# Kernel optimization log

Measured on AMD Instinct MI355X. Metric: run time of the kernel, lower is better.

## Reference

```python
import jax, jax.numpy as jnp
import numpy as np

N, E, B = 50000, 800000, 64
F0, H, C = 8, 2, 64          # node feat dim, heads, per-head out dim
OBS, MH, NA = 128, 256, 16   # obs dim, mlp hidden, n_actions
NEG_SLOPE = 0.2


def setup_inputs() -> dict:
    key = jax.random.key(0)
    ks = jax.random.split(key, 30)
    p = lambda k, shape: (jax.random.normal(k, shape, dtype=jnp.float32) * 0.1)
    inp = {
        "obs": jax.random.normal(ks[0], (B, OBS), dtype=jnp.float32),
        "node_features": jax.random.normal(ks[1], (N, F0), dtype=jnp.float32),
        "edge_index": jax.random.randint(ks[2], (2, E), 0, N, dtype=jnp.int32),
        "batch": jnp.sort(jax.random.randint(ks[3], (N,), 0, B, dtype=jnp.int32)),
        # GAT layer 0: in=F0 -> heads=H, out=C, concat
        "W0": p(ks[4], (F0, H * C)), "a_src0": p(ks[5], (H, C)), "a_dst0": p(ks[6], (H, C)), "b0": p(ks[7], (H * C,)),
        # GAT layer 1: in=H*C -> heads=H, out=C, concat
        "W1": p(ks[8], (H * C, H * C)), "a_src1": p(ks[9], (H, C)), "a_dst1": p(ks[10], (H, C)), "b1": p(ks[11], (H * C,)),
        # GAT layer 2: in=H*C -> heads=1, out=C, no concat
        "W2": p(ks[12], (H * C, C)), "a_src2": p(ks[13], (1, C)), "a_dst2": p(ks[14], (1, C)), "b2": p(ks[15], (C,)),
        # MLP head: combined = C + OBS
        "Ws1": p(ks[16], (C + OBS, MH)), "bs1": p(ks[17], (MH,)),
        "ln_g": jnp.ones((MH,), jnp.float32), "ln_b": jnp.zeros((MH,), jnp.float32),
        "Ws2": p(ks[18], (MH, MH)), "bs2": p(ks[19], (MH,)),
        "Wa": p(ks[20], (MH, NA)), "ba": p(ks[21], (NA,)),
        "Wc": p(ks[22], (MH, 1)), "bc": p(ks[23], (1,)),
    }
    return inp


def gat_layer(x, src, dst, W, a_src, a_dst, bias, heads, out_dim, concat):
    n = x.shape[0]
    h = (x @ W).reshape(n, heads, out_dim)                     # [N,H,C]
    alpha_s = jnp.einsum("nhc,hc->nh", h, a_src)               # [N,H]
    alpha_d = jnp.einsum("nhc,hc->nh", h, a_dst)
    e = jax.nn.leaky_relu(alpha_s[src] + alpha_d[dst], NEG_SLOPE)  # [E,H]
    # scatter-softmax over incoming edges of each dst node (stable)
    emax = jax.ops.segment_max(e, dst, num_segments=n)
    ex = jnp.exp(e - emax[dst])
    denom = jax.ops.segment_sum(ex, dst, num_segments=n)
    alpha = ex / (denom[dst] + 1e-16)                          # [E,H]
    msg = h[src] * alpha[..., None]                            # [E,H,C]
    out = jax.ops.segment_sum(msg, dst, num_segments=n)        # [N,H,C]
    out = out.reshape(n, heads * out_dim) if concat else out.mean(axis=1)
    return out + bias


def reference(obs, node_features, edge_index, batch,
              W0, a_src0, a_dst0, b0, W1, a_src1, a_dst1, b1,
              W2, a_src2, a_dst2, b2,
              Ws1, bs1, ln_g, ln_b, Ws2, bs2, Wa, ba, Wc, bc):
    n = node_features.shape[0]
    # PyG GATConv default add_self_loops=True
    loop = jnp.arange(n, dtype=edge_index.dtype)
    src = jnp.concatenate([edge_index[0], loop])
    dst = jnp.concatenate([edge_index[1], loop])

    x = node_features
    x = jax.nn.elu(gat_layer(x, src, dst, W0, a_src0, a_dst0, b0, H, C, True))
    x = jax.nn.elu(gat_layer(x, src, dst, W1, a_src1, a_dst1, b1, H, C, True))
    x = gat_layer(x, src, dst, W2, a_src2, a_dst2, b2, 1, C, False)

    # global mean pool over graphs
    counts = jax.ops.segment_sum(jnp.ones((n,), x.dtype), batch, num_segments=B)
    pooled = jax.ops.segment_sum(x, batch, num_segments=B) / jnp.maximum(counts, 1.0)[:, None]

    combined = jnp.concatenate([pooled, obs], axis=-1)         # [B, C+OBS]
    h = combined @ Ws1 + bs1
    mu = h.mean(-1, keepdims=True)
    var = ((h - mu) ** 2).mean(-1, keepdims=True)
    h = (h - mu) / jnp.sqrt(var + 1e-5) * ln_g + ln_b
    h = jax.nn.relu(h)
    h = jax.nn.relu(h @ Ws2 + bs2)
    logits = h @ Wa + ba
    value = (h @ Wc + bc).squeeze(-1)
    return logits, value
```

## Files before the change

### kernel.cpp

```cpp
#include <hip/hip_runtime.h>
#include <math.h>


#define LRELU(x) ((x) > 0.f ? (x) : 0.2f * (x))

typedef short bf16x8 __attribute__((ext_vector_type(8)));
typedef unsigned short u16x8 __attribute__((ext_vector_type(8)));
typedef float f32x4 __attribute__((ext_vector_type(4)));
typedef float f32x2 __attribute__((ext_vector_type(2)));

__device__ __forceinline__ unsigned short f2bf(float f) {
    unsigned int u = __float_as_uint(f);
    u = (u + 0x7fffu + ((u >> 16) & 1u)) >> 16;
    return (unsigned short)u;
}
__device__ __forceinline__ float bf2f(unsigned short u) {
    return __uint_as_float((unsigned int)u << 16);
}
__device__ __forceinline__ unsigned char f2fp8(float f) {
    return (unsigned char)(__builtin_amdgcn_cvt_pk_fp8_f32(f, f, 0, false) & 0xff);
}
__device__ __forceinline__ f32x2 fp8pair(unsigned int u) {
    return __builtin_amdgcn_cvt_pk_f32_fp8(u, false);
}


__global__ __launch_bounds__(256) void hist_t0_kernel(
    const int* __restrict__ dst, int* __restrict__ histT,
    int e, int G1, int NB, int n, int hist_blocks, int t0_blocks, int wp_blocks,
    const float* __restrict__ x, const float* __restrict__ W,
    const float* __restrict__ a_src, const float* __restrict__ a_dst,
    unsigned char* __restrict__ h, float* __restrict__ as_o,
    float* __restrict__ ad_o,
    const float* __restrict__ W1, const float* __restrict__ W2,
    unsigned short* __restrict__ Wf1, unsigned short* __restrict__ Wf2,
    const int* __restrict__ batch, int* __restrict__ gstart, int nGraphs) {
    __shared__ unsigned int hist[256];
    __shared__ float xs[2][8][8];
    const int t = threadIdx.x;
    if ((int)blockIdx.x < hist_blocks) {
        hist[t] = 0;
        __syncthreads();
        int base = blockIdx.x * 2048 + t * 8;
        int d[8];
        if (base + 8 <= e) {
            int4 x0 = *(const int4*)(dst + base);
            int4 x1 = *(const int4*)(dst + base + 4);
            d[0] = x0.x; d[1] = x0.y; d[2] = x0.z; d[3] = x0.w;
            d[4] = x1.x; d[5] = x1.y; d[6] = x1.z; d[7] = x1.w;
        } else {
#pragma unroll
            for (int j = 0; j < 8; j++) {
                int ij = base + j;
                d[j] = (ij < e) ? dst[ij] : -1;
            }
        }
#pragma unroll
        for (int j = 0; j < 8; j++) {
            if (d[j] >= 0) atomicAdd(&hist[d[j] >> 8], 1u);
        }
        __syncthreads();
        if (t < NB) histT[t * G1 + blockIdx.x] = (int)hist[t];
        return;
    }
    if ((int)blockIdx.x < hist_blocks + t0_blocks) {
        const int bid2 = blockIdx.x - hist_blocks;
        const int tid = t & 127;
        const int half = t >> 7;
        const int node0 = bid2 * 16 + half * 8;

        for (int idx = tid; idx < 64; idx += 128) {
            int ni = idx >> 3, k = idx & 7;
            int ng = node0 + ni;
            xs[half][ni][k] = (ng < n) ? x[(size_t)ng * 8 + k] : 0.f;
        }
        __syncthreads();

        float acc[8];
#pragma unroll
        for (int i = 0; i < 8; i++) acc[i] = 0.f;
#pragma unroll
        for (int k = 0; k < 8; k++) {
            float wk = W[k * 128 + tid];
#pragma unroll
            for (int i = 0; i < 8; i++) acc[i] += xs[half][i][k] * wk;
        }

        const int lane = tid & 63;
        const int head = tid >> 6;
        const int pos = 2 * lane + head;
        const float av = a_src[tid];
        const float dv = a_dst[tid];
#pragma unroll
        for (int i = 0; i < 8; i++) {
            int ng = node0 + i;
            if (ng >= n) break;
            h[(size_t)ng * 128 + pos] = f2fp8(acc[i]);
            float ps = acc[i] * av, pd = acc[i] * dv;
            for (int off = 32; off; off >>= 1) {
                ps += __shfl_xor(ps, off, 64);
                pd += __shfl_xor(pd, off, 64);
            }
            if (lane == 0) {
                as_o[ng * 2 + head] = ps;
                ad_o[ng * 2 + head] = pd;
            }
        }
        return;
    }
    if ((int)blockIdx.x < hist_blocks + t0_blocks + wp_blocks) {
        const int n1 = 8 * 4 * 64;
        const int n2 = 4 * 4 * 64;
        int gid = (blockIdx.x - hist_blocks - t0_blocks) * 256 + t;
        if (gid < n1) {
            int idx = gid;
            int lane = idx & 63, ts = idx >> 6;
            int s = ts & 3, tt = ts >> 2;
            int quad = lane >> 4, cn = lane & 15;
#pragma unroll
            for (int j = 0; j < 8; j++)
                Wf1[idx * 8 + j] = f2bf(W1[(s * 32 + quad * 8 + j) * 128 + tt * 16 + cn]);
        } else if (gid < n1 + n2) {
            int idx = gid - n1;
            int lane = idx & 63, ts = idx >> 6;
            int s = ts & 3, tt = ts >> 2;
            int quad = lane >> 4, cn = lane & 15;
#pragma unroll
            for (int j = 0; j < 8; j++)
                Wf2[idx * 8 + j] = f2bf(W2[(s * 32 + quad * 8 + j) * 64 + tt * 16 + cn]);
        }
        return;
    }
    int gid = (blockIdx.x - hist_blocks - t0_blocks - wp_blocks) * 256 + t;
    if (gid < n) {
        int bi = batch[gid];
        if (gid == 0) {
            for (int g = 0; g <= bi; g++) gstart[g] = 0;
        } else {
            int bp = batch[gid - 1];
            if (bi != bp)
                for (int g = bp + 1; g <= bi; g++) gstart[g] = gid;
        }
        if (gid == n - 1) {
            for (int g = bi + 1; g <= nGraphs; g++) gstart[g] = n;
        }
    }
}


__global__ __launch_bounds__(256) void scan2_block_kernel(
    const int* __restrict__ in, int* __restrict__ out,
    int* __restrict__ blockSums, int len) {
    __shared__ int lds[256];
    int t = threadIdx.x;
    int i0 = blockIdx.x * 512 + 2 * t;
    int v0 = (i0 < len) ? in[i0] : 0;
    int v1 = (i0 + 1 < len) ? in[i0 + 1] : 0;
    int s = v0 + v1;
    lds[t] = s;
    __syncthreads();
    for (int off = 1; off < 256; off <<= 1) {
        int u = (t >= off) ? lds[t - off] : 0;
        __syncthreads();
        lds[t] += u;
        __syncthreads();
    }
    int base = lds[t] - s;
    if (i0 < len) out[i0] = base;
    if (i0 + 1 < len) out[i0 + 1] = base + v0;
    if (t == 255) blockSums[blockIdx.x] = lds[255];
}

__global__ __launch_bounds__(256) void scan2_finalize_kernel(
    int* __restrict__ out, const int* __restrict__ blockSums, int len, int nb) {
    __shared__ int lds[256];
    int t = threadIdx.x;
    int v = (t < nb) ? blockSums[t] : 0;
    lds[t] = v;
    __syncthreads();
    for (int off = 1; off < 256; off <<= 1) {
        int u = (t >= off) ? lds[t - off] : 0;
        __syncthreads();
        lds[t] += u;
        __syncthreads();
    }
    const int bid = blockIdx.x;
    const int base = (bid > 0) ? lds[bid - 1] : 0;
    const int total = lds[nb - 1];
    int i0 = bid * 512 + 2 * t;
#pragma unroll
    for (int q = 0; q < 2; q++) {
        int i = i0 + q;
        if (i < len) out[i] += base;
        else if (i == len) out[len] = total;
    }
}


__global__ __launch_bounds__(256) void bucket_scatter_kernel(
    const int* __restrict__ src, const int* __restrict__ dst,
    const int* __restrict__ offs, int* __restrict__ esrc,
    unsigned char* __restrict__ dsub8, int e, int G1, int NB) {
    __shared__ unsigned int hist[256];
    __shared__ int baseL[256];
    const int t = threadIdx.x;
    hist[t] = 0;
    if (t < NB) baseL[t] = offs[t * G1 + blockIdx.x];
    __syncthreads();
    int base = blockIdx.x * 2048 + t * 8;
    int d[8], s[8];
    if (base + 8 <= e) {
        int4 d0 = *(const int4*)(dst + base);
        int4 d1 = *(const int4*)(dst + base + 4);
        int4 s0 = *(const int4*)(src + base);
        int4 s1 = *(const int4*)(src + base + 4);
        d[0] = d0.x; d[1] = d0.y; d[2] = d0.z; d[3] = d0.w;
        d[4] = d1.x; d[5] = d1.y; d[6] = d1.z; d[7] = d1.w;
        s[0] = s0.x; s[1] = s0.y; s[2] = s0.z; s[3] = s0.w;
        s[4] = s1.x; s[5] = s1.y; s[6] = s1.z; s[7] = s1.w;
    } else {
#pragma unroll
        for (int j = 0; j < 8; j++) {
            int ij = base + j;
            bool v = ij < e;
            d[j] = v ? dst[ij] : -1;
            s[j] = v ? src[ij] : 0;
        }
    }
    unsigned lr[8];
#pragma unroll
    for (int j = 0; j < 8; j++) {
        lr[j] = (d[j] >= 0) ? atomicAdd(&hist[d[j] >> 8], 1u) : 0u;
    }
#pragma unroll
    for (int j = 0; j < 8; j++) {
        if (d[j] >= 0) {
            int pos = baseL[d[j] >> 8] + (int)lr[j];
            esrc[pos] = s[j];
            dsub8[pos] = (unsigned char)(d[j] & 255);
        }
    }
}


__global__ __launch_bounds__(256) void bucket_csr_kernel(
    const int* __restrict__ offs, const unsigned char* __restrict__ dsub8,
    const int* __restrict__ esrc, int* __restrict__ row_ptr,
    int* __restrict__ col, int G1, int n) {
    __shared__ unsigned int cnt[256];
    __shared__ int rp[256];
    int t = threadIdx.x;
    int b = blockIdx.x;
    cnt[t] = 0;
    __syncthreads();
    int bs = offs[b * G1];
    int be = offs[(b + 1) * G1];
    for (int i = bs + t; i < be; i += 256) {
        atomicAdd(&cnt[dsub8[i]], 1u);
    }
    __syncthreads();
    int v = (int)cnt[t];
    rp[t] = v;
    __syncthreads();
    for (int off = 1; off < 256; off <<= 1) {
        int u = (t >= off) ? rp[t - off] : 0;
        __syncthreads();
        rp[t] += u;
        __syncthreads();
    }
    int excl = rp[t] - v;
    int node = b * 256 + t;
    if (node <= n) row_ptr[node] = bs + excl;
    __syncthreads();
    cnt[t] = (unsigned)excl;
    __syncthreads();
    for (int i = bs + t; i < be; i += 256) {
        int sub = dsub8[i];
        unsigned r = atomicAdd(&cnt[sub], 1u);
        col[bs + (int)r] = esrc[i];
    }
}

template <int OUT, int HEADS>
__device__ __forceinline__ int hpos8(int c) {
    return (HEADS == 2) ? (2 * (c & 63) + (c >> 6)) : c;
}


template <int OUT, int HEADS>
__global__ __launch_bounds__(256) void transform_mfma_kernel(
    const unsigned short* __restrict__ xb, const unsigned short* __restrict__ Wf,
    const float* __restrict__ a_src, const float* __restrict__ a_dst,
    unsigned char* __restrict__ h, float* __restrict__ as_o, float* __restrict__ ad_o,
    int n) {
    constexpr int T = OUT / 16, S = 4;
    const int w = threadIdx.x >> 6, lane = threadIdx.x & 63;
    const int node0 = (blockIdx.x * 4 + w) * 16;
    if (node0 >= n) return;
    const int quad = lane >> 4, col = lane & 15;

    const int arow = node0 + col;
    const bool aok = arow < n;
    bf16x8 a[S];
    const unsigned short* xrow = xb + (size_t)arow * 128 + quad * 8;
#pragma unroll
    for (int s = 0; s < S; s++) {
        bf16x8 z = {0, 0, 0, 0, 0, 0, 0, 0};
        a[s] = aok ? *(const bf16x8*)(xrow + s * 32) : z;
    }

    f32x4 acc[T];
#pragma unroll
    for (int t = 0; t < T; t++) acc[t] = (f32x4){0.f, 0.f, 0.f, 0.f};

#pragma unroll
    for (int s = 0; s < S; s++) {
#pragma unroll
        for (int t = 0; t < T; t++) {
            bf16x8 b = *(const bf16x8*)(Wf + ((size_t)(t * S + s) * 64 + lane) * 8);
            acc[t] = __builtin_amdgcn_mfma_f32_16x16x32_bf16(a[s], b, acc[t], 0, 0, 0);
        }
    }

#pragma unroll
    for (int t = 0; t < T; t++) {
        int pos = hpos8<OUT, HEADS>(t * 16 + col);
#pragma unroll
        for (int r = 0; r < 4; r++) {
            int m = node0 + quad * 4 + r;
            if (m < n) h[(size_t)m * OUT + pos] = f2fp8(acc[t][r]);
        }
    }

#pragma unroll
    for (int r = 0; r < 4; r++) {
        float s0 = 0.f, s1 = 0.f, d0 = 0.f, d1 = 0.f;
#pragma unroll
        for (int t = 0; t < T; t++) {
            float av = a_src[t * 16 + col];
            float dv = a_dst[t * 16 + col];
            float v = acc[t][r];
            if (HEADS == 2 && t >= T / 2) { s1 += v * av; d1 += v * dv; }
            else                          { s0 += v * av; d0 += v * dv; }
        }
        for (int off = 8; off; off >>= 1) {
            s0 += __shfl_xor(s0, off, 64);
            d0 += __shfl_xor(d0, off, 64);
            if (HEADS == 2) {
                s1 += __shfl_xor(s1, off, 64);
                d1 += __shfl_xor(d1, off, 64);
            }
        }
        int m = node0 + quad * 4 + r;
        if (m < n) {
            if (HEADS == 2) {
                if (col == 0)      { as_o[m * 2] = s0;     ad_o[m * 2] = d0; }
                else if (col == 1) { as_o[m * 2 + 1] = s1; ad_o[m * 2 + 1] = d1; }
            } else {
                if (col == 0) { as_o[m] = s0; ad_o[m] = d0; }
            }
        }
    }
}


template <int ACT>
__global__ __launch_bounds__(256) void agg2_kernel(
    const int* __restrict__ row_ptr, const int* __restrict__ col,
    const unsigned char* __restrict__ h, const float2* __restrict__ as2,
    const float2* __restrict__ ad2, const float* __restrict__ bias,
    unsigned short* __restrict__ out, int n) {
    __shared__ float w0l[4][2][32], w1l[4][2][32];
    __shared__ unsigned sofl[4][2][32];
    const int w = threadIdx.x >> 6;
    const int lane = threadIdx.x & 63;
    const int half = lane >> 5, l = lane & 31;
    const int node = blockIdx.x * 8 + w * 2 + half;
    const bool active = node < n;

    int beg = 0, deg = 0;
    float2 adv = make_float2(0.f, 0.f);
    float den0 = 0.f, den1 = 0.f;
    float a0 = 0.f, a1 = 0.f, a2 = 0.f, a3 = 0.f;
    if (active) {
        beg = row_ptr[node];
        deg = row_ptr[node + 1] - beg;
        adv = ad2[node];
        float2 avs = as2[node];
        float w0s = __expf(LRELU(avs.x + adv.x));
        float w1s = __expf(LRELU(avs.y + adv.y));
        unsigned us = *(const unsigned*)(h + ((size_t)node << 7) + 4 * l);
        f32x2 p0 = fp8pair(us & 0xffffu);
        f32x2 p1 = fp8pair(us >> 16);
        a0 = w0s * p0.x; a1 = w1s * p0.y;
        a2 = w0s * p1.x; a3 = w1s * p1.y;
        den0 = w0s; den1 = w1s;
    }
    int dmax = deg;
    for (int off = 32; off; off >>= 1) dmax = max(dmax, __shfl_xor(dmax, off, 64));

    for (int base = 0; base < dmax; base += 32) {
        int cnt = deg - base;
        cnt = cnt < 0 ? 0 : (cnt > 32 ? 32 : cnt);
        float w0 = 0.f, w1 = 0.f;
        unsigned so = 0;
        if (l < cnt) {
            int s = col[beg + base + l];
            float2 av = as2[s];
            w0 = __expf(LRELU(av.x + adv.x));
            w1 = __expf(LRELU(av.y + adv.y));
            so = (unsigned)s << 7;
        }
        float t0 = w0, t1 = w1;
        for (int off = 16; off; off >>= 1) {
            t0 += __shfl_xor(t0, off, 64);
            t1 += __shfl_xor(t1, off, 64);
        }
        den0 += t0; den1 += t1;
        w0l[w][half][l] = w0;
        w1l[w][half][l] = w1;
        sofl[w][half][l] = so;

        int jmax = dmax - base;
        jmax = jmax > 32 ? 32 : jmax;
        for (int j = 0; j < jmax; j += 8) {
            unsigned u[8];
#pragma unroll
            for (int k = 0; k < 8; k++) {
                unsigned so_k = sofl[w][half][j + k];
                u[k] = *(const unsigned*)(h + so_k + 4 * l);
            }
            float W0[8], W1[8];
#pragma unroll
            for (int k = 0; k < 8; k++) {
                W0[k] = w0l[w][half][j + k];
                W1[k] = w1l[w][half][j + k];
            }
#pragma unroll
            for (int k = 0; k < 8; k++) {
                f32x2 p0 = fp8pair(u[k] & 0xffffu);
                f32x2 p1 = fp8pair(u[k] >> 16);
                a0 += W0[k] * p0.x; a1 += W1[k] * p0.y;
                a2 += W0[k] * p1.x; a3 += W1[k] * p1.y;
            }
        }
    }

    if (active) {
        float2 bA = *(const float2*)(bias + 2 * l);
        float2 bB = *(const float2*)(bias + 64 + 2 * l);
        float r0 = 1.f / (den0 + 1e-16f), r1 = 1.f / (den1 + 1e-16f);
        float o0 = a0 * r0 + bA.x;
        float o1 = a1 * r1 + bB.x;
        float o2 = a2 * r0 + bA.y;
        float o3 = a3 * r1 + bB.y;
        if (ACT) {
            o0 = o0 > 0.f ? o0 : expm1f(o0);
            o1 = o1 > 0.f ? o1 : expm1f(o1);
            o2 = o2 > 0.f ? o2 : expm1f(o2);
            o3 = o3 > 0.f ? o3 : expm1f(o3);
        }
        unsigned h0 = (unsigned)f2bf(o0) | ((unsigned)f2bf(o2) << 16);
        unsigned h1 = (unsigned)f2bf(o1) | ((unsigned)f2bf(o3) << 16);
        *(unsigned*)(out + (size_t)node * 128 + 2 * l) = h0;
        *(unsigned*)(out + (size_t)node * 128 + 64 + 2 * l) = h1;
    }
}


__global__ __launch_bounds__(256) void agg1_kernel(
    const int* __restrict__ row_ptr, const int* __restrict__ col,
    const unsigned char* __restrict__ h, const float* __restrict__ as1,
    const float* __restrict__ ad1, const float* __restrict__ bias,
    unsigned short* __restrict__ out, int n) {
    __shared__ float wl[4][2][32];
    __shared__ unsigned sofl[4][2][32];
    const int w = threadIdx.x >> 6;
    const int lane = threadIdx.x & 63;
    const int half = lane >> 5, l = lane & 31;
    const int node = blockIdx.x * 8 + w * 2 + half;
    const bool active = node < n;

    int beg = 0, deg = 0;
    float adv = 0.f, den = 0.f, a0 = 0.f, a2 = 0.f;
    if (active) {
        beg = row_ptr[node];
        deg = row_ptr[node + 1] - beg;
        adv = ad1[node];
        float ws = __expf(LRELU(as1[node] + adv));
        unsigned us = *(const unsigned short*)(h + ((size_t)node << 6) + 2 * l);
        f32x2 p = fp8pair(us);
        a0 = ws * p.x;
        a2 = ws * p.y;
        den = ws;
    }
    int dmax = deg;
    for (int off = 32; off; off >>= 1) dmax = max(dmax, __shfl_xor(dmax, off, 64));

    for (int base = 0; base < dmax; base += 32) {
        int cnt = deg - base;
        cnt = cnt < 0 ? 0 : (cnt > 32 ? 32 : cnt);
        float w0 = 0.f;
        unsigned so = 0;
        if (l < cnt) {
            int s = col[beg + base + l];
            w0 = __expf(LRELU(as1[s] + adv));
            so = (unsigned)s << 6;
        }
        float t = w0;
        for (int off = 16; off; off >>= 1) t += __shfl_xor(t, off, 64);
        den += t;
        wl[w][half][l] = w0;
        sofl[w][half][l] = so;

        int jmax = dmax - base;
        jmax = jmax > 32 ? 32 : jmax;
        for (int j = 0; j < jmax; j += 8) {
            unsigned u[8];
#pragma unroll
            for (int k = 0; k < 8; k++) {
                unsigned so_k = sofl[w][half][j + k];
                u[k] = *(const unsigned short*)(h + so_k + 2 * l);
            }
            float W0[8];
#pragma unroll
            for (int k = 0; k < 8; k++) W0[k] = wl[w][half][j + k];
#pragma unroll
            for (int k = 0; k < 8; k++) {
                f32x2 p = fp8pair(u[k]);
                a0 += W0[k] * p.x;
                a2 += W0[k] * p.y;
            }
        }
    }

    if (active) {
        float2 bA = *(const float2*)(bias + 2 * l);
        float r = 1.f / (den + 1e-16f);
        float o0 = a0 * r + bA.x;
        float o2 = a2 * r + bA.y;
        unsigned hv = (unsigned)f2bf(o0) | ((unsigned)f2bf(o2) << 16);
        *(unsigned*)(out + (size_t)node * 64 + 2 * l) = hv;
    }
}


__global__ __launch_bounds__(512) void mlp_kernel(
    const unsigned short* __restrict__ xbuf, const int* __restrict__ gstart,
    const float* __restrict__ obs,
    const float* __restrict__ Ws1, const float* __restrict__ bs1,
    const float* __restrict__ ln_g, const float* __restrict__ ln_b,
    const float* __restrict__ Ws2, const float* __restrict__ bs2,
    const float* __restrict__ Wa, const float* __restrict__ ba,
    const float* __restrict__ Wc, const float* __restrict__ bc,
    float* __restrict__ out_logits, float* __restrict__ out_value) {
    int b = blockIdx.x;
    int t = threadIdx.x;
    __shared__ float comb[192];
    __shared__ float red[512];
    __shared__ float red2[8][64];
    __shared__ float hs[256];

    const int gs = gstart[b];
    const int ge = gstart[b + 1];

    {
        const int w = t >> 6, lane = t & 63;
        const int rg = w * 8 + (lane >> 3);
        const int sub = lane & 7;
        float acc[8];
#pragma unroll
        for (int j = 0; j < 8; j++) acc[j] = 0.f;
        for (int i = gs + rg; i < ge; i += 64) {
            u16x8 v = *(const u16x8*)(xbuf + (size_t)i * 64 + sub * 8);
#pragma unroll
            for (int j = 0; j < 8; j++) acc[j] += bf2f(v[j]);
        }
#pragma unroll
        for (int off = 8; off <= 32; off <<= 1) {
#pragma unroll
            for (int j = 0; j < 8; j++) acc[j] += __shfl_xor(acc[j], off, 64);
        }
        if (lane < 8) {
#pragma unroll
            for (int j = 0; j < 8; j++) red2[w][lane * 8 + j] = acc[j];
        }
    }
    __syncthreads();
    {
        float cdiv = fmaxf((float)(ge - gs), 1.f);
        if (t < 64) {
            float s = 0.f;
#pragma unroll
            for (int w = 0; w < 8; w++) s += red2[w][t];
            comb[t] = s / cdiv;
        } else if (t < 192) {
            comb[t] = obs[b * 128 + (t - 64)];
        }
    }
    __syncthreads();

    const int t256 = t & 255;
    const int khalf = t >> 8;

    {
        float accA = 0.f, accB = 0.f;
        int k0 = khalf * 96;
#pragma unroll 4
        for (int k = k0; k < k0 + 96; k += 2) {
            accA += comb[k] * Ws1[k * 256 + t256];
            accB += comb[k + 1] * Ws1[(k + 1) * 256 + t256];
        }
        red[t] = accA + accB;
    }
    __syncthreads();
    float acc = 0.f;
    if (t < 256) acc = bs1[t] + red[t] + red[t + 256];
    __syncthreads();

    red[t] = (t < 256) ? acc : 0.f;
    __syncthreads();
    for (int off = 128; off; off >>= 1) {
        if (t < off) red[t] += red[t + off];
        __syncthreads();
    }
    float mu = red[0] / 256.f;
    __syncthreads();
    float d = acc - mu;
    red[t] = (t < 256) ? d * d : 0.f;
    __syncthreads();
    for (int off = 128; off; off >>= 1) {
        if (t < off) red[t] += red[t + off];
        __syncthreads();
    }
    float var = red[0] / 256.f;
    if (t < 256) {
        float hn = d * rsqrtf(var + 1e-5f) * ln_g[t] + ln_b[t];
        hs[t] = hn > 0.f ? hn : 0.f;
    }
    __syncthreads();

    {
        float a2A = 0.f, a2B = 0.f;
        int k0 = khalf * 128;
#pragma unroll 4
        for (int k = k0; k < k0 + 128; k += 2) {
            a2A += hs[k] * Ws2[k * 256 + t256];
            a2B += hs[k + 1] * Ws2[(k + 1) * 256 + t256];
        }
        red[t] = a2A + a2B;
    }
    __syncthreads();
    float acc2 = 0.f;
    if (t < 256) {
        acc2 = bs2[t] + red[t] + red[t + 256];
        acc2 = acc2 > 0.f ? acc2 : 0.f;
    }
    __syncthreads();
    if (t < 256) hs[t] = acc2;
    __syncthreads();

    {
        int o = t & 15, ck = t >> 4;
        float p = 0.f;
#pragma unroll
        for (int k = 0; k < 8; k++)
            p += hs[ck * 8 + k] * Wa[(ck * 8 + k) * 16 + o];
        red[t] = p;
    }
    __syncthreads();
    for (int off = 16; off >= 1; off >>= 1) {
        if ((t >> 4) < off) red[t] += red[t + off * 16];
        __syncthreads();
    }
    if (t < 16) out_logits[b * 16 + t] = red[t] + ba[t];
    __syncthreads();

    red[t] = (t < 256) ? hs[t] * Wc[t] : 0.f;
    __syncthreads();
    for (int off = 256; off; off >>= 1) {
        if (t < off) red[t] += red[t + off];
        __syncthreads();
    }
    if (t == 0) out_value[b] = red[0] + bc[0];
}


extern "C" void kernel_launch(void* const* d_in, const int* in_sizes, int n_in,
                              void* d_out, int out_size, void* d_ws, size_t ws_size,
                              hipStream_t stream) {
    const float* obs    = (const float*)d_in[0];
    const float* nf     = (const float*)d_in[1];
    const int*   ei     = (const int*)d_in[2];
    const int*   batch  = (const int*)d_in[3];
    const float* W0     = (const float*)d_in[4];
    const float* a_src0 = (const float*)d_in[5];
    const float* a_dst0 = (const float*)d_in[6];
    const float* b0     = (const float*)d_in[7];
    const float* W1     = (const float*)d_in[8];
    const float* a_src1 = (const float*)d_in[9];
    const float* a_dst1 = (const float*)d_in[10];
    const float* b1     = (const float*)d_in[11];
    const float* W2     = (const float*)d_in[12];
    const float* a_src2 = (const float*)d_in[13];
    const float* a_dst2 = (const float*)d_in[14];
    const float* b2     = (const float*)d_in[15];
    const float* Ws1    = (const float*)d_in[16];
    const float* bs1    = (const float*)d_in[17];
    const float* ln_g   = (const float*)d_in[18];
    const float* ln_b   = (const float*)d_in[19];
    const float* Ws2    = (const float*)d_in[20];
    const float* bs2    = (const float*)d_in[21];
    const float* Wa     = (const float*)d_in[22];
    const float* ba     = (const float*)d_in[23];
    const float* Wc     = (const float*)d_in[24];
    const float* bc     = (const float*)d_in[25];

    const int N = in_sizes[3];
    const int E = in_sizes[2] / 2;
    const int B = in_sizes[0] / 128;
    const int* src = ei;
    const int* dstp = ei + E;

    char* p = (char*)d_ws;
    auto alloc = [&](size_t bytes) -> void* {
        void* r = (void*)p;
        p += (bytes + 255) & ~(size_t)255;
        return r;
    };
    const int G1 = (E + 2047) / 2048;
    const int NB = (N + 255) >> 8;
    const int L  = NB * G1;
    int*   row_ptr   = (int*)alloc((size_t)(N + 1) * 4);
    int*   col       = (int*)alloc((size_t)E * 4);
    int*   esrc      = (int*)alloc((size_t)E * 4);
    unsigned char* dsub8 = (unsigned char*)alloc((size_t)E);
    int*   histT     = (int*)alloc((size_t)L * 4);
    int*   offs      = (int*)alloc((size_t)(L + 1) * 4);
    unsigned char* hbuf = (unsigned char*)alloc((size_t)N * 128);
    unsigned short* xb = (unsigned short*)alloc((size_t)N * 128 * 2);
    unsigned short* xbuf = (unsigned short*)alloc((size_t)N * 64 * 2);
    float* as_       = (float*)alloc((size_t)N * 2 * 4);
    float* ad_       = (float*)alloc((size_t)N * 2 * 4);
    unsigned short* Wf1 = (unsigned short*)alloc((size_t)8 * 4 * 64 * 8 * 2);
    unsigned short* Wf2 = (unsigned short*)alloc((size_t)4 * 4 * 64 * 8 * 2);
    int* gstart      = (int*)alloc((size_t)(B + 1) * 4);
    int* blockSums = (int*)xb;

    float* out_logits = (float*)d_out;
    float* out_value  = out_logits + (size_t)B * 16;

    int t0_blocks = (N + 15) / 16;
    int wp_blocks = (8 * 4 * 64 + 4 * 4 * 64 + 255) / 256;
    int gb_blocks = (N + 255) / 256;
    hist_t0_kernel<<<G1 + t0_blocks + wp_blocks + gb_blocks, 256, 0, stream>>>(
        dstp, histT, E, G1, NB, N, G1, t0_blocks, wp_blocks,
        nf, W0, a_src0, a_dst0, hbuf, as_, ad_,
        W1, W2, Wf1, Wf2, batch, gstart, B);

    int nbA = (L + 511) / 512;
    scan2_block_kernel<<<nbA, 256, 0, stream>>>(histT, offs, blockSums, L);
    scan2_finalize_kernel<<<(L + 1 + 511) / 512, 256, 0, stream>>>(offs, blockSums, L, nbA);

    bucket_scatter_kernel<<<G1, 256, 0, stream>>>(src, dstp, offs, esrc, dsub8, E, G1, NB);
    bucket_csr_kernel<<<NB, 256, 0, stream>>>(offs, dsub8, esrc, row_ptr, col, G1, N);

    agg2_kernel<1><<<(N + 7) / 8, 256, 0, stream>>>(
        row_ptr, col, hbuf, (const float2*)as_, (const float2*)ad_, b0, xb, N);

    transform_mfma_kernel<128, 2><<<(N + 63) / 64, 256, 0, stream>>>(
        xb, Wf1, a_src1, a_dst1, hbuf, as_, ad_, N);
    agg2_kernel<1><<<(N + 7) / 8, 256, 0, stream>>>(
        row_ptr, col, hbuf, (const float2*)as_, (const float2*)ad_, b1, xb, N);

    transform_mfma_kernel<64, 1><<<(N + 63) / 64, 256, 0, stream>>>(
        xb, Wf2, a_src2, a_dst2, hbuf, as_, ad_, N);
    agg1_kernel<<<(N + 7) / 8, 256, 0, stream>>>(
        row_ptr, col, hbuf, as_, ad_, b2, xbuf, N);

    mlp_kernel<<<B, 512, 0, stream>>>(xbuf, gstart, obs, Ws1, bs1, ln_g, ln_b,
                                      Ws2, bs2, Wa, ba, Wc, bc,
                                      out_logits, out_value);
}
```

Measured before the change: 262.1 us.

## Fuse GAT aggregation with next layer's MFMA transform via shared-memory tile

Merges the two-head aggregation kernel with the following layer's MFMA linear transform and attention-score computation. Each 512-thread block aggregates 16 nodes into a bf16 tile in LDS, then runs the MFMA projection and writes fp8 features plus per-head attention logits for the next layer. Ping-pong feature and score buffers avoid read/write hazards. This removes the bf16 intermediate round trip to global memory and two kernel launches, at the cost of more LDS, block-wide syncs and idle waves during the transform phase (only OUT/16 waves do MFMA).

```diff
diff --git a/kernel.cpp b/kernel.cpp
--- a/kernel.cpp
+++ b/kernel.cpp
@@ -22,6 +22,11 @@
 }
 __device__ __forceinline__ f32x2 fp8pair(unsigned int u) {
     return __builtin_amdgcn_cvt_pk_f32_fp8(u, false);
+}
+
+template <int OUT, int HEADS>
+__device__ __forceinline__ int hpos8(int c) {
+    return (HEADS == 2) ? (2 * (c & 63) + (c >> 6)) : c;
 }
 
 
@@ -281,101 +286,25 @@
     }
 }
 
-template <int OUT, int HEADS>
-__device__ __forceinline__ int hpos8(int c) {
-    return (HEADS == 2) ? (2 * (c & 63) + (c >> 6)) : c;
-}
-
-
-template <int OUT, int HEADS>
-__global__ __launch_bounds__(256) void transform_mfma_kernel(
-    const unsigned short* __restrict__ xb, const unsigned short* __restrict__ Wf,
-    const float* __restrict__ a_src, const float* __restrict__ a_dst,
-    unsigned char* __restrict__ h, float* __restrict__ as_o, float* __restrict__ ad_o,
-    int n) {
-    constexpr int T = OUT / 16, S = 4;
-    const int w = threadIdx.x >> 6, lane = threadIdx.x & 63;
-    const int node0 = (blockIdx.x * 4 + w) * 16;
-    if (node0 >= n) return;
-    const int quad = lane >> 4, col = lane & 15;
-
-    const int arow = node0 + col;
-    const bool aok = arow < n;
-    bf16x8 a[S];
-    const unsigned short* xrow = xb + (size_t)arow * 128 + quad * 8;
-#pragma unroll
-    for (int s = 0; s < S; s++) {
-        bf16x8 z = {0, 0, 0, 0, 0, 0, 0, 0};
-        a[s] = aok ? *(const bf16x8*)(xrow + s * 32) : z;
-    }
-
-    f32x4 acc[T];
-#pragma unroll
-    for (int t = 0; t < T; t++) acc[t] = (f32x4){0.f, 0.f, 0.f, 0.f};
-
-#pragma unroll
-    for (int s = 0; s < S; s++) {
-#pragma unroll
-        for (int t = 0; t < T; t++) {
-            bf16x8 b = *(const bf16x8*)(Wf + ((size_t)(t * S + s) * 64 + lane) * 8);
-            acc[t] = __builtin_amdgcn_mfma_f32_16x16x32_bf16(a[s], b, acc[t], 0, 0, 0);
-        }
-    }
-
-#pragma unroll
-    for (int t = 0; t < T; t++) {
-        int pos = hpos8<OUT, HEADS>(t * 16 + col);
-#pragma unroll
-        for (int r = 0; r < 4; r++) {
-            int m = node0 + quad * 4 + r;
-            if (m < n) h[(size_t)m * OUT + pos] = f2fp8(acc[t][r]);
-        }
-    }
-
-#pragma unroll
-    for (int r = 0; r < 4; r++) {
-        float s0 = 0.f, s1 = 0.f, d0 = 0.f, d1 = 0.f;
-#pragma unroll
-        for (int t = 0; t < T; t++) {
-            float av = a_src[t * 16 + col];
-            float dv = a_dst[t * 16 + col];
-            float v = acc[t][r];
-            if (HEADS == 2 && t >= T / 2) { s1 += v * av; d1 += v * dv; }
-            else                          { s0 += v * av; d0 += v * dv; }
-        }
-        for (int off = 8; off; off >>= 1) {
-            s0 += __shfl_xor(s0, off, 64);
-            d0 += __shfl_xor(d0, off, 64);
-            if (HEADS == 2) {
-                s1 += __shfl_xor(s1, off, 64);
-                d1 += __shfl_xor(d1, off, 64);
-            }
-        }
-        int m = node0 + quad * 4 + r;
-        if (m < n) {
-            if (HEADS == 2) {
-                if (col == 0)      { as_o[m * 2] = s0;     ad_o[m * 2] = d0; }
-                else if (col == 1) { as_o[m * 2 + 1] = s1; ad_o[m * 2 + 1] = d1; }
-            } else {
-                if (col == 0) { as_o[m] = s0; ad_o[m] = d0; }
-            }
-        }
-    }
-}
-
-
-template <int ACT>
-__global__ __launch_bounds__(256) void agg2_kernel(
+
+template <int OUT2, int HEADS2>
+__global__ __launch_bounds__(512) void agg2t_kernel(
     const int* __restrict__ row_ptr, const int* __restrict__ col,
     const unsigned char* __restrict__ h, const float2* __restrict__ as2,
     const float2* __restrict__ ad2, const float* __restrict__ bias,
-    unsigned short* __restrict__ out, int n) {
-    __shared__ float w0l[4][2][32], w1l[4][2][32];
-    __shared__ unsigned sofl[4][2][32];
+    const unsigned short* __restrict__ Wf, const float* __restrict__ aN_src,
+    const float* __restrict__ aN_dst, unsigned char* __restrict__ hN,
+    float* __restrict__ asN, float* __restrict__ adN, int n) {
+    __shared__ float w0l[8][2][32], w1l[8][2][32];
+    __shared__ unsigned sofl[8][2][32];
+    __shared__ unsigned short xs[16][136];
+    __shared__ float asP[16][8], adP[16][8];
     const int w = threadIdx.x >> 6;
     const int lane = threadIdx.x & 63;
     const int half = lane >> 5, l = lane & 31;
-    const int node = blockIdx.x * 8 + w * 2 + half;
+    const int node0 = blockIdx.x * 16;
+    const int mloc = w * 2 + half;
+    const int node = node0 + mloc;
     const bool active = node < n;
 
     int beg = 0, deg = 0;
@@ -454,16 +383,67 @@
         float o1 = a1 * r1 + bB.x;
         float o2 = a2 * r0 + bA.y;
         float o3 = a3 * r1 + bB.y;
-        if (ACT) {
-            o0 = o0 > 0.f ? o0 : expm1f(o0);
-            o1 = o1 > 0.f ? o1 : expm1f(o1);
-            o2 = o2 > 0.f ? o2 : expm1f(o2);
-            o3 = o3 > 0.f ? o3 : expm1f(o3);
-        }
-        unsigned h0 = (unsigned)f2bf(o0) | ((unsigned)f2bf(o2) << 16);
-        unsigned h1 = (unsigned)f2bf(o1) | ((unsigned)f2bf(o3) << 16);
-        *(unsigned*)(out + (size_t)node * 128 + 2 * l) = h0;
-        *(unsigned*)(out + (size_t)node * 128 + 64 + 2 * l) = h1;
+        o0 = o0 > 0.f ? o0 : expm1f(o0);
+        o1 = o1 > 0.f ? o1 : expm1f(o1);
+        o2 = o2 > 0.f ? o2 : expm1f(o2);
+        o3 = o3 > 0.f ? o3 : expm1f(o3);
+        *(unsigned*)&xs[mloc][2 * l] = (unsigned)f2bf(o0) | ((unsigned)f2bf(o2) << 16);
+        *(unsigned*)&xs[mloc][64 + 2 * l] = (unsigned)f2bf(o1) | ((unsigned)f2bf(o3) << 16);
+    } else {
+        *(unsigned*)&xs[mloc][2 * l] = 0;
+        *(unsigned*)&xs[mloc][64 + 2 * l] = 0;
+    }
+    __syncthreads();
+
+    constexpr int T2 = OUT2 / 16, S = 4;
+    const int quad = lane >> 4, colc = lane & 15;
+    if (w < T2) {
+        bf16x8 a[S];
+#pragma unroll
+        for (int s = 0; s < S; s++)
+            a[s] = *(const bf16x8*)&xs[colc][quad * 8 + s * 32];
+        f32x4 acc = (f32x4){0.f, 0.f, 0.f, 0.f};
+#pragma unroll
+        for (int s = 0; s < S; s++) {
+            bf16x8 b = *(const bf16x8*)(Wf + ((size_t)(w * S + s) * 64 + lane) * 8);
+            acc = __builtin_amdgcn_mfma_f32_16x16x32_bf16(a[s], b, acc, 0, 0, 0);
+        }
+        const int pos = hpos8<OUT2, HEADS2>(w * 16 + colc);
+#pragma unroll
+        for (int r = 0; r < 4; r++) {
+            int m = node0 + quad * 4 + r;
+            if (m < n) hN[(size_t)m * OUT2 + pos] = f2fp8(acc[r]);
+        }
+        const float av = aN_src[w * 16 + colc];
+        const float dv = aN_dst[w * 16 + colc];
+#pragma unroll
+        for (int r = 0; r < 4; r++) {
+            float sp = acc[r] * av, dp = acc[r] * dv;
+            for (int off = 8; off; off >>= 1) {
+                sp += __shfl_xor(sp, off, 64);
+                dp += __shfl_xor(dp, off, 64);
+            }
+            if (colc == 0) {
+                asP[quad * 4 + r][w] = sp;
+                adP[quad * 4 + r][w] = dp;
+            }
+        }
+    }
+    __syncthreads();
+    const int tt = threadIdx.x;
+    if (tt < 16 * HEADS2) {
+        int m = tt & 15, head = tt >> 4;
+        int node2 = node0 + m;
+        if (node2 < n) {
+            float s = 0.f, d = 0.f;
+#pragma unroll
+            for (int ww = 0; ww < 4; ww++) {
+                s += asP[m][head * 4 + ww];
+                d += adP[m][head * 4 + ww];
+            }
+            asN[node2 * HEADS2 + head] = s;
+            adN[node2 * HEADS2 + head] = d;
+        }
     }
 }
 
@@ -737,15 +717,19 @@
     unsigned char* dsub8 = (unsigned char*)alloc((size_t)E);
     int*   histT     = (int*)alloc((size_t)L * 4);
     int*   offs      = (int*)alloc((size_t)(L + 1) * 4);
-    unsigned char* hbuf = (unsigned char*)alloc((size_t)N * 128);
-    unsigned short* xb = (unsigned short*)alloc((size_t)N * 128 * 2);
+    unsigned char* hbufA = (unsigned char*)alloc((size_t)N * 128);
+    unsigned char* hbufB = (unsigned char*)alloc((size_t)N * 128);
     unsigned short* xbuf = (unsigned short*)alloc((size_t)N * 64 * 2);
-    float* as_       = (float*)alloc((size_t)N * 2 * 4);
-    float* ad_       = (float*)alloc((size_t)N * 2 * 4);
+    float* as0       = (float*)alloc((size_t)N * 2 * 4);
+    float* ad0       = (float*)alloc((size_t)N * 2 * 4);
+    float* as1       = (float*)alloc((size_t)N * 2 * 4);
+    float* ad1       = (float*)alloc((size_t)N * 2 * 4);
+    float* as2v      = (float*)alloc((size_t)N * 4);
+    float* ad2v      = (float*)alloc((size_t)N * 4);
     unsigned short* Wf1 = (unsigned short*)alloc((size_t)8 * 4 * 64 * 8 * 2);
     unsigned short* Wf2 = (unsigned short*)alloc((size_t)4 * 4 * 64 * 8 * 2);
     int* gstart      = (int*)alloc((size_t)(B + 1) * 4);
-    int* blockSums = (int*)xb;
+    int* blockSums   = (int*)alloc((size_t)1024 * 4);
 
     float* out_logits = (float*)d_out;
     float* out_value  = out_logits + (size_t)B * 16;
@@ -755,7 +739,7 @@
     int gb_blocks = (N + 255) / 256;
     hist_t0_kernel<<<G1 + t0_blocks + wp_blocks + gb_blocks, 256, 0, stream>>>(
         dstp, histT, E, G1, NB, N, G1, t0_blocks, wp_blocks,
-        nf, W0, a_src0, a_dst0, hbuf, as_, ad_,
+        nf, W0, a_src0, a_dst0, hbufA, as0, ad0,
         W1, W2, Wf1, Wf2, batch, gstart, B);
 
     int nbA = (L + 511) / 512;
@@ -765,18 +749,16 @@
     bucket_scatter_kernel<<<G1, 256, 0, stream>>>(src, dstp, offs, esrc, dsub8, E, G1, NB);
     bucket_csr_kernel<<<NB, 256, 0, stream>>>(offs, dsub8, esrc, row_ptr, col, G1, N);
 
-    agg2_kernel<1><<<(N + 7) / 8, 256, 0, stream>>>(
-        row_ptr, col, hbuf, (const float2*)as_, (const float2*)ad_, b0, xb, N);
-
-    transform_mfma_kernel<128, 2><<<(N + 63) / 64, 256, 0, stream>>>(
-        xb, Wf1, a_src1, a_dst1, hbuf, as_, ad_, N);
-    agg2_kernel<1><<<(N + 7) / 8, 256, 0, stream>>>(
-        row_ptr, col, hbuf, (const float2*)as_, (const float2*)ad_, b1, xb, N);
-
-    transform_mfma_kernel<64, 1><<<(N + 63) / 64, 256, 0, stream>>>(
-        xb, Wf2, a_src2, a_dst2, hbuf, as_, ad_, N);
+    agg2t_kernel<128, 2><<<(N + 15) / 16, 512, 0, stream>>>(
+        row_ptr, col, hbufA, (const float2*)as0, (const float2*)ad0, b0,
+        Wf1, a_src1, a_dst1, hbufB, as1, ad1, N);
+
+    agg2t_kernel<64, 1><<<(N + 15) / 16, 512, 0, stream>>>(
+        row_ptr, col, hbufB, (const float2*)as1, (const float2*)ad1, b1,
+        Wf2, a_src2, a_dst2, hbufA, as2v, ad2v, N);
+
     agg1_kernel<<<(N + 7) / 8, 256, 0, stream>>>(
-        row_ptr, col, hbuf, as_, ad_, b2, xbuf, N);
+        row_ptr, col, hbufA, as2v, ad2v, b2, xbuf, N);
 
     mlp_kernel<<<B, 512, 0, stream>>>(xbuf, gstart, obs, Ws1, bs1, ln_g, ln_b,
                                       Ws2, bs2, Wa, ba, Wc, bc,
```

After: 259.5 us. About the same (-1.0%).
